# Kernel tuning notes

Measured on AMD Instinct MI355X. Metric: run time of the kernel, lower is better.

## Reference

```python
import jax, jax.numpy as jnp
import numpy as np
import math

B, T, C = 4, 2048, 1024
N_HEAD = 16
HEAD = C // N_HEAD  # 64
ROPE_BASE = 10000.0


def rotate_half(x):
    x1, x2 = x[..., : x.shape[-1] // 2], x[..., x.shape[-1] // 2:]
    return jnp.concatenate((-x2, x1), axis=-1)


def rope_cos_sin(seq_len, dim, dtype=jnp.float32):
    inv_freq = 1.0 / (ROPE_BASE ** (jnp.arange(0, dim, 2, dtype=jnp.float32) / dim))
    t = jnp.arange(seq_len, dtype=jnp.float32)
    freqs = jnp.einsum('i,j->ij', t, inv_freq)          # [T, dim/2]
    emb = jnp.concatenate((freqs, freqs), axis=-1)       # [T, dim]
    return jnp.cos(emb).astype(dtype), jnp.sin(emb).astype(dtype)


def setup_inputs() -> dict:
    key = jax.random.key(0)
    ks = jax.random.split(key, 5)
    s_in = 1.0 / math.sqrt(C)
    return {
        'x': jax.random.normal(ks[0], (B, T, C), dtype=jnp.float32),
        'W_qkv': jax.random.normal(ks[1], (C, 3 * C), dtype=jnp.float32) * s_in,
        'b_qkv': jnp.zeros((3 * C,), dtype=jnp.float32),
        'W_proj': jax.random.normal(ks[2], (C, C), dtype=jnp.float32) * s_in,
        'b_proj': jnp.zeros((C,), dtype=jnp.float32),
    }


def reference(x, W_qkv, b_qkv, W_proj, b_proj):
    b, t, c = x.shape
    qkv = x @ W_qkv + b_qkv                               # [B,T,3C]
    q, k, v = jnp.split(qkv, 3, axis=-1)
    # [B,T,C] -> [B,H,T,hd]
    def to_heads(u):
        return u.reshape(b, t, N_HEAD, HEAD).transpose(0, 2, 1, 3)
    q, k, v = to_heads(q), to_heads(k), to_heads(v)
    # RoPE
    cos, sin = rope_cos_sin(t, HEAD, x.dtype)             # [T,hd]
    cos = cos[None, None]; sin = sin[None, None]
    q = q * cos + rotate_half(q) * sin
    k = k * cos + rotate_half(k) * sin
    # naive causal attention (materializes [B,H,T,T] like the original)
    att = jnp.einsum('bhqd,bhkd->bhqk', q, k) * (1.0 / math.sqrt(HEAD))
    causal = jnp.tril(jnp.ones((t, t), dtype=bool))
    att = jnp.where(causal[None, None], att, -jnp.inf)
    att = jax.nn.softmax(att, axis=-1)
    y = jnp.einsum('bhqk,bhkd->bhqd', att, v)             # [B,H,T,hd]
    y = y.transpose(0, 2, 1, 3).reshape(b, t, c)
    return y @ W_proj + b_proj
```

## Files before the change

### kernel.cpp

```cpp
#include <hip/hip_runtime.h>
#include <stdint.h>

#define B_  4
#define T_  2048
#define C_  1024
#define NH_ 16
#define HD_ 64
#define BH_ (B_*NH_)
#define M_  (B_*T_)

using f32x4  = __attribute__((ext_vector_type(4))) float;
using f32x16 = __attribute__((ext_vector_type(16))) float;
using bf16x8 = __attribute__((ext_vector_type(8))) short;

__device__ __forceinline__ unsigned short f2bf(float x) {
  union { float f; uint32_t u; } v; v.f = x;
  uint32_t u = v.u;
  return (unsigned short)((u + 0x7FFFu + ((u >> 16) & 1u)) >> 16);
}

__device__ __forceinline__ uint32_t cvtpk(float a, float b) {
  uint32_t r;
  asm("v_cvt_pk_bf16_f32 %0, %1, %2" : "=v"(r) : "v"(a), "v"(b));
  return r;
}

__device__ __forceinline__ void gload16(const void* g, void* l) {
  __builtin_amdgcn_global_load_lds(
      (const __attribute__((address_space(1))) void*)g,
      (__attribute__((address_space(3))) void*)l, 16, 0, 0);
}

#define BAR() do { asm volatile("" ::: "memory"); __builtin_amdgcn_s_barrier(); \
                   asm volatile("" ::: "memory"); } while (0)
#define VMC(N) asm volatile("s_waitcnt vmcnt(" #N ")" ::: "memory")

__global__ __launch_bounds__(256)
void k_prep(const float* __restrict__ x,      unsigned short* __restrict__ xb,
            const float* __restrict__ Wqkv,   unsigned short* __restrict__ WqkvT,
            const float* __restrict__ Wproj,  unsigned short* __restrict__ WprojT,
            float* __restrict__ cosT, float* __restrict__ sinT) {
  __shared__ float tile[32][33];
  const int blk = blockIdx.x;
  const int tid = threadIdx.x;
  if (blk < 8192) {
    int i = (blk * 256 + tid) * 4;
    float4 v = *(const float4*)(x + i);
    ushort4 o;
    o.x = f2bf(v.x); o.y = f2bf(v.y); o.z = f2bf(v.z); o.w = f2bf(v.w);
    *(ushort4*)(xb + i) = o;
    return;
  }
  const int tx = tid & 31, ty = tid >> 5;
  if (blk < 12288) {
    const float* W; unsigned short* WT; int N, local;
    if (blk < 11264) { W = Wqkv;  WT = WqkvT;  N = 3*C_; local = blk - 8192; }
    else             { W = Wproj; WT = WprojT; N = C_;   local = blk - 11264; }
    const int NT = N / 32;
    const int bx = local % NT, by = local / NT;
    #pragma unroll
    for (int i = 0; i < 32; i += 8)
      tile[ty + i][tx] = W[(size_t)(by*32 + ty + i) * N + bx*32 + tx];
    __syncthreads();
    #pragma unroll
    for (int i = 0; i < 32; i += 8)
      WT[(size_t)(bx*32 + ty + i) * C_ + by*32 + tx] = f2bf(tile[tx][ty + i]);
    return;
  }
  {
    int t = (blk - 12288) * 8 + ty;
    float inv = expf(-(float)tx * (9.210340371976184f / 32.0f));
    float f = (float)t * inv;
    cosT[t*32 + tx] = cosf(f);
    sinT[t*32 + tx] = sinf(f);
  }
}

template<int N, int K, int EPI>
__global__ __launch_bounds__(256)
void k_gemm(const unsigned short* __restrict__ Ag,
            const unsigned short* __restrict__ BT,
            const float* __restrict__ bias,
            const float* __restrict__ cosT,
            const float* __restrict__ sinT,
            unsigned short* __restrict__ Qh,
            unsigned short* __restrict__ Kh,
            unsigned short* __restrict__ VhT,
            float* __restrict__ outF) {
  __shared__ alignas(16) unsigned short As[2][128*64];
  __shared__ alignas(16) unsigned short Bs[2][128*64];
  const int tid  = threadIdx.x;
  const int lane = tid & 63;
  const int wv   = tid >> 6;
  const int wm   = wv >> 1, wn = wv & 1;
  const int l15  = lane & 15, l4 = lane >> 4;
  constexpr int GN = (N == 3072) ? 6 : 8;
  const int xcd = (int)blockIdx.x & 7;
  const int loc = (int)blockIdx.x >> 3;
  const int sub = loc / (8*GN);
  const int wit = loc % (8*GN);
  const int m0  = (xcd*8 + wit / GN) * 128;
  const int n0  = (sub*GN + wit % GN) * 128;

  f32x4 acc[4][4] = {};

  const int g0 = l4 ^ (l15 & 7);
  const int g1 = (4 + l4) ^ (l15 & 7);
  const int rowA = wm*64 + l15, rowB = wn*64 + l15;
  const unsigned short* aRd0k0 = &As[0][rowA*64 + g0*8];
  const unsigned short* aRd0k1 = &As[0][rowA*64 + g1*8];
  const unsigned short* aRd1k0 = &As[1][rowA*64 + g0*8];
  const unsigned short* aRd1k1 = &As[1][rowA*64 + g1*8];
  const unsigned short* bRd0k0 = &Bs[0][rowB*64 + g0*8];
  const unsigned short* bRd0k1 = &Bs[0][rowB*64 + g1*8];
  const unsigned short* bRd1k0 = &Bs[1][rowB*64 + g0*8];
  const unsigned short* bRd1k1 = &Bs[1][rowB*64 + g1*8];

  const int srow = wv*8 + (lane >> 3);
  const int sg   = (lane & 7) ^ ((lane >> 3) & 7);
  const int voff = srow*K + sg*8;
  const int aUni = m0*K, bUni = n0*K;
  const int ldsD = wv*512;

#define STG(BUF, KT) do { \
  const int _u = (KT)*64; \
  _Pragma("unroll") for (int it = 0; it < 4; ++it) { \
    gload16(Ag + (aUni + it*(32*K) + _u) + voff, (void*)(&As[BUF][it*2048 + ldsD])); \
    gload16(BT + (bUni + it*(32*K) + _u) + voff, (void*)(&Bs[BUF][it*2048 + ldsD])); \
  } \
} while (0)

#define CMP(AK0, AK1, BK0, BK1) do { \
  bf16x8 afr[4][2], bfr[4][2]; \
  _Pragma("unroll") for (int mi = 0; mi < 4; ++mi) { \
    afr[mi][0] = *(const bf16x8*)((AK0) + mi*1024); \
    afr[mi][1] = *(const bf16x8*)((AK1) + mi*1024); \
    bfr[mi][0] = *(const bf16x8*)((BK0) + mi*1024); \
    bfr[mi][1] = *(const bf16x8*)((BK1) + mi*1024); \
  } \
  __builtin_amdgcn_s_setprio(1); \
  _Pragma("unroll") for (int ks = 0; ks < 2; ++ks) \
  _Pragma("unroll") for (int mi = 0; mi < 4; ++mi) \
  _Pragma("unroll") for (int ni = 0; ni < 4; ++ni) \
    acc[mi][ni] = __builtin_amdgcn_mfma_f32_16x16x32_bf16( \
        afr[mi][ks], bfr[ni][ks], acc[mi][ni], 0, 0, 0); \
  __builtin_amdgcn_s_setprio(0); \
} while (0)

  STG(0, 0);
  #pragma unroll 1
  for (int i = 0; i < K/128; ++i) {
    STG(1, 2*i + 1);
    VMC(8);
    BAR();
    CMP(aRd0k0, aRd0k1, bRd0k0, bRd0k1);
    BAR();
    if (i + 1 < K/128) {
      STG(0, 2*i + 2);
      VMC(8);
    } else {
      VMC(0);
    }
    BAR();
    CMP(aRd1k0, aRd1k1, bRd1k0, bRd1k1);
    BAR();
  }
#undef STG
#undef CMP

  if (EPI == 0) {
    const int ncol = n0 + wn*64;
    const int part = ncol >> 10;
    const int hid  = (ncol & 1023) >> 6;
    unsigned short* dstQK = (part == 0) ? Qh : Kh;
    #pragma unroll
    for (int mi = 0; mi < 4; ++mi) {
      #pragma unroll
      for (int j = 0; j < 4; ++j) {
        int row = m0 + wm*64 + mi*16 + l4*4 + j;
        int bb = row >> 11, tt = row & 2047;
        if (part < 2) {
          size_t base = ((size_t)((bb*NH_ + hid) * T_ + tt)) * HD_;
          #pragma unroll
          for (int ni = 0; ni < 2; ++ni) {
            int d = ni*16 + l15;
            float a1 = acc[mi][ni][j]     + bias[ncol + d];
            float a2 = acc[mi][ni + 2][j] + bias[ncol + d + 32];
            float cv = cosT[tt*32 + d], sv = sinT[tt*32 + d];
            float o1 = a1*cv - a2*sv;
            float o2 = a2*cv + a1*sv;
            if (part == 0) { o1 *= 0.18033688011112042f; o2 *= 0.18033688011112042f; }
            dstQK[base + d]      = f2bf(o1);
            dstQK[base + d + 32] = f2bf(o2);
          }
        } else {
          #pragma unroll
          for (int ni = 0; ni < 4; ++ni) {
            int d = ni*16 + l15;
            float av = acc[mi][ni][j] + bias[ncol + d];
            VhT[((size_t)((bb*NH_ + hid) * HD_ + d)) * T_ + tt] = f2bf(av);
          }
        }
      }
    }
  } else {
    #pragma unroll
    for (int mi = 0; mi < 4; ++mi)
      #pragma unroll
      for (int ni = 0; ni < 4; ++ni)
        #pragma unroll
        for (int j = 0; j < 4; ++j) {
          int row = m0 + wm*64 + mi*16 + l4*4 + j;
          int col = n0 + wn*64 + ni*16 + l15;
          outF[(size_t)row * N + col] = acc[mi][ni][j] + bias[col];
        }
  }
}

#define LDW 72
__global__ __launch_bounds__(256, 3)
void k_attn(const unsigned short* __restrict__ Qh,
            const unsigned short* __restrict__ Kh,
            const unsigned short* __restrict__ VhT,
            unsigned short* __restrict__ Y) {
  __shared__ alignas(16) unsigned short Ks[2][64*LDW];
  __shared__ alignas(16) unsigned short Vs[2][64*LDW];
  const int tid  = threadIdx.x;
  const int lane = tid & 63;
  const int wv   = tid >> 6;
  const int l31  = lane & 31;
  const int h    = lane >> 5;
  const int bh   = blockIdx.x & 63;
  const int qb   = 15 - (blockIdx.x >> 6);
  const int r32  = qb*128 + wv*32;
  const int nt   = 2*qb + 2;
  const int qg   = r32 + l31;

  bf16x8 qf[4];
  #pragma unroll
  for (int i = 0; i < 4; ++i)
    qf[i] = *(const bf16x8*)(Qh + ((size_t)(bh*T_ + qg))*HD_ + i*16 + h*8);

  float m_r = -1e30f, l_r = 0.f;
  f32x16 o[2] = {};

  const int srow  = tid >> 3;
  const int sslot = tid & 7;
  const unsigned short* kSrc0 = Kh  + ((size_t)(bh*T_ + srow))*HD_ + sslot*8;
  const unsigned short* kSrc1 = Kh  + ((size_t)(bh*T_ + 32 + srow))*HD_ + sslot*8;
  const unsigned short* vSrc0 = VhT + ((size_t)(bh*HD_ + srow))*T_ + sslot*8;
  const unsigned short* vSrc1 = VhT + ((size_t)(bh*HD_ + 32 + srow))*T_ + sslot*8;
  const int wOff0 = srow*LDW + sslot*8;
  const int wOff1 = (32 + srow)*LDW + sslot*8;

  uint4 kr0, kr1, vr0, vr1;
  auto ldg = [&](int jt) {
    kr0 = *(const uint4*)(kSrc0 + (size_t)jt*64*HD_);
    kr1 = *(const uint4*)(kSrc1 + (size_t)jt*64*HD_);
    vr0 = *(const uint4*)(vSrc0 + jt*64);
    vr1 = *(const uint4*)(vSrc1 + jt*64);
  };
  auto wst = [&](int buf) {
    *(uint4*)(&Ks[buf][wOff0]) = kr0;
    *(uint4*)(&Ks[buf][wOff1]) = kr1;
    *(uint4*)(&Vs[buf][wOff0]) = vr0;
    *(uint4*)(&Vs[buf][wOff1]) = vr1;
  };

  ldg(0); wst(0);
  __syncthreads();
  int cur = 0;

  for (int jt = 0; jt < nt; ++jt) {
    const bool pf = (jt + 1 < nt);
    if (pf) ldg(jt + 1);

    if (jt*64 <= r32 + 31) {
      const unsigned short* kb_ = &Ks[cur][l31*LDW + h*8];
      const unsigned short* vb_ = &Vs[cur][l31*LDW + h*8];

      f32x16 s[2] = {f32x16{0}, f32x16{0}};
      __builtin_amdgcn_s_setprio(1);
      #pragma unroll
      for (int kb = 0; kb < 2; ++kb)
        #pragma unroll
        for (int i = 0; i < 4; ++i) {
          bf16x8 kf = *(const bf16x8*)(kb_ + kb*32*LDW + i*16);
          s[kb] = __builtin_amdgcn_mfma_f32_32x32x16_bf16(kf, qf[i], s[kb], 0, 0, 0);
        }
      __builtin_amdgcn_s_setprio(0);

      float p[2][16];
      const bool diag = (jt + 1)*64 > r32;
      #pragma unroll
      for (int kb = 0; kb < 2; ++kb)
        #pragma unroll
        for (int r = 0; r < 16; ++r) {
          float v = s[kb][r];
          if (diag) {
            int key = jt*64 + kb*32 + (r & 3) + 8*(r >> 2) + 4*h;
            v = (key > qg) ? -1e30f : v;
          }
          p[kb][r] = v;
        }

      float mx[16];
      #pragma unroll
      for (int r = 0; r < 16; ++r) mx[r] = fmaxf(p[0][r], p[1][r]);
      #pragma unroll
      for (int st = 8; st > 0; st >>= 1)
        #pragma unroll
        for (int r = 0; r < 8; ++r)
          if (r < st) mx[r] = fmaxf(mx[r], mx[r + st]);
      float tm = fmaxf(mx[0], __shfl_xor(mx[0], 32));

      if (!__all(tm <= m_r + 8.0f)) {
        float mn = fmaxf(m_r, tm);
        float scale = exp2f(m_r - mn);
        m_r = mn;
        l_r *= scale;
        #pragma unroll
        for (int dblk = 0; dblk < 2; ++dblk)
          #pragma unroll
          for (int r = 0; r < 16; ++r)
            o[dblk][r] *= scale;
      }

      #pragma unroll
      for (int kb = 0; kb < 2; ++kb)
        #pragma unroll
        for (int r = 0; r < 16; ++r)
          p[kb][r] = exp2f(p[kb][r] - m_r);

      float sm[16];
      #pragma unroll
      for (int r = 0; r < 16; ++r) sm[r] = p[0][r] + p[1][r];
      #pragma unroll
      for (int st = 8; st > 0; st >>= 1)
        #pragma unroll
        for (int r = 0; r < 8; ++r)
          if (r < st) sm[r] += sm[r + st];
      l_r += sm[0] + __shfl_xor(sm[0], 32);

      #pragma unroll
      for (int kb = 0; kb < 2; ++kb) {
        uint32_t a01 = cvtpk(p[kb][0],  p[kb][1]);
        uint32_t a23 = cvtpk(p[kb][2],  p[kb][3]);
        uint32_t a45 = cvtpk(p[kb][4],  p[kb][5]);
        uint32_t a67 = cvtpk(p[kb][6],  p[kb][7]);
        uint32_t b01 = cvtpk(p[kb][8],  p[kb][9]);
        uint32_t b23 = cvtpk(p[kb][10], p[kb][11]);
        uint32_t b45 = cvtpk(p[kb][12], p[kb][13]);
        uint32_t b67 = cvtpk(p[kb][14], p[kb][15]);
        uint32_t s1 = h ? a01 : a45, s2 = h ? a23 : a67;
        uint32_t s3 = h ? b01 : b45, s4 = h ? b23 : b67;
        uint32_t x1 = __shfl_xor(s1, 32), x2 = __shfl_xor(s2, 32);
        uint32_t x3 = __shfl_xor(s3, 32), x4 = __shfl_xor(s4, 32);
        union { bf16x8 v; uint32_t d[4]; } f0, f1;
        f0.d[0] = h ? x1 : a01;  f0.d[1] = h ? x2 : a23;
        f0.d[2] = h ? a45 : x1;  f0.d[3] = h ? a67 : x2;
        f1.d[0] = h ? x3 : b01;  f1.d[1] = h ? x4 : b23;
        f1.d[2] = h ? b45 : x3;  f1.d[3] = h ? b67 : x4;

        __builtin_amdgcn_s_setprio(1);
        #pragma unroll
        for (int koff = 0; koff < 2; ++koff) {
          bf16x8 pf = koff ? f1.v : f0.v;
          #pragma unroll
          for (int dblk = 0; dblk < 2; ++dblk) {
            bf16x8 vf = *(const bf16x8*)(vb_ + dblk*32*LDW + kb*32 + koff*16);
            o[dblk] = __builtin_amdgcn_mfma_f32_32x32x16_bf16(vf, pf, o[dblk], 0, 0, 0);
          }
        }
        __builtin_amdgcn_s_setprio(0);
      }
    }

    if (pf) wst(cur ^ 1);
    __syncthreads();
    cur ^= 1;
  }

  int b = bh >> 4, hd = bh & 15;
  float rinv = 1.0f / l_r;
  unsigned short* yrow = Y + ((size_t)(b*T_ + r32 + l31))*C_ + hd*64;
  #pragma unroll
  for (int dblk = 0; dblk < 2; ++dblk)
    #pragma unroll
    for (int g2 = 0; g2 < 4; ++g2) {
      ushort4 o4;
      o4.x = f2bf(o[dblk][g2*4 + 0] * rinv);
      o4.y = f2bf(o[dblk][g2*4 + 1] * rinv);
      o4.z = f2bf(o[dblk][g2*4 + 2] * rinv);
      o4.w = f2bf(o[dblk][g2*4 + 3] * rinv);
      *(ushort4*)(yrow + dblk*32 + g2*8 + 4*h) = o4;
    }
}


extern "C" void kernel_launch(void* const* d_in, const int* in_sizes, int n_in,
                              void* d_out, int out_size, void* d_ws, size_t ws_size,
                              hipStream_t stream) {
  const float* x      = (const float*)d_in[0];
  const float* W_qkv  = (const float*)d_in[1];
  const float* b_qkv  = (const float*)d_in[2];
  const float* W_proj = (const float*)d_in[3];
  const float* b_proj = (const float*)d_in[4];
  float* out = (float*)d_out;

  char* ws = (char*)d_ws;
  size_t off = 0;
  auto alloc = [&](size_t bytes) {
    void* p = ws + off; off += (bytes + 255) & ~(size_t)255; return p;
  };
  unsigned short* xb     = (unsigned short*)alloc((size_t)M_ * C_ * 2);
  unsigned short* WqkvT  = (unsigned short*)alloc((size_t)3 * C_ * C_ * 2);
  unsigned short* WprojT = (unsigned short*)alloc((size_t)C_ * C_ * 2);
  unsigned short* Qh     = (unsigned short*)alloc((size_t)M_ * C_ * 2);
  unsigned short* Kh     = (unsigned short*)alloc((size_t)M_ * C_ * 2);
  unsigned short* VhT    = (unsigned short*)alloc((size_t)M_ * C_ * 2);
  float* cosT = (float*)alloc((size_t)T_ * 32 * 4);
  float* sinT = (float*)alloc((size_t)T_ * 32 * 4);
  unsigned short* Y = xb;

  k_prep<<<dim3(12544), 256, 0, stream>>>(x, xb, W_qkv, WqkvT, W_proj, WprojT,
                                          cosT, sinT);

  k_gemm<3*C_, C_, 0><<<dim3(1536), 256, 0, stream>>>(
      xb, WqkvT, b_qkv, cosT, sinT, Qh, Kh, VhT, nullptr);

  k_attn<<<dim3(T_/128 * BH_), 256, 0, stream>>>(Qh, Kh, VhT, Y);

  k_gemm<C_, C_, 1><<<dim3(512), 256, 0, stream>>>(
      Y, WprojT, b_proj, nullptr, nullptr, nullptr, nullptr, nullptr, out);
}
```

Measured before the change: 188.4 us.

## Enlarge attention KV tile to 128 keys per iteration

```diff
diff --git a/kernel.cpp b/kernel.cpp
--- a/kernel.cpp
+++ b/kernel.cpp
@@ -217,14 +217,15 @@
   }
 }
 
-#define LDW 72
-__global__ __launch_bounds__(256, 3)
+#define LDWK 72
+#define LDWV 136
+__global__ __launch_bounds__(256, 2)
 void k_attn(const unsigned short* __restrict__ Qh,
             const unsigned short* __restrict__ Kh,
             const unsigned short* __restrict__ VhT,
             unsigned short* __restrict__ Y) {
-  __shared__ alignas(16) unsigned short Ks[2][64*LDW];
-  __shared__ alignas(16) unsigned short Vs[2][64*LDW];
+  __shared__ alignas(16) unsigned short Ks[2][128*LDWK];
+  __shared__ alignas(16) unsigned short Vs[2][64*LDWV];
   const int tid  = threadIdx.x;
   const int lane = tid & 63;
   const int wv   = tid >> 6;
@@ -233,7 +234,7 @@
   const int bh   = blockIdx.x & 63;
   const int qb   = 15 - (blockIdx.x >> 6);
   const int r32  = qb*128 + wv*32;
-  const int nt   = 2*qb + 2;
+  const int nt   = qb + 1;
   const int qg   = r32 + l31;
 
   bf16x8 qf[4];
@@ -246,25 +247,27 @@
 
   const int srow  = tid >> 3;
   const int sslot = tid & 7;
-  const unsigned short* kSrc0 = Kh  + ((size_t)(bh*T_ + srow))*HD_ + sslot*8;
-  const unsigned short* kSrc1 = Kh  + ((size_t)(bh*T_ + 32 + srow))*HD_ + sslot*8;
-  const unsigned short* vSrc0 = VhT + ((size_t)(bh*HD_ + srow))*T_ + sslot*8;
-  const unsigned short* vSrc1 = VhT + ((size_t)(bh*HD_ + 32 + srow))*T_ + sslot*8;
-  const int wOff0 = srow*LDW + sslot*8;
-  const int wOff1 = (32 + srow)*LDW + sslot*8;
-
-  uint4 kr0, kr1, vr0, vr1;
+  const unsigned short* kSrc = Kh + ((size_t)(bh*T_ + srow))*HD_ + sslot*8;
+  const int kOff = srow*LDWK + sslot*8;
+  const int vd    = tid >> 2;
+  const int vslot = tid & 3;
+  const unsigned short* vSrc = VhT + ((size_t)(bh*HD_ + vd))*T_ + vslot*8;
+  const int vOff = vd*LDWV + vslot*8;
+
+  uint4 kr[4], vr[4];
   auto ldg = [&](int jt) {
-    kr0 = *(const uint4*)(kSrc0 + (size_t)jt*64*HD_);
-    kr1 = *(const uint4*)(kSrc1 + (size_t)jt*64*HD_);
-    vr0 = *(const uint4*)(vSrc0 + jt*64);
-    vr1 = *(const uint4*)(vSrc1 + jt*64);
+    #pragma unroll
+    for (int c = 0; c < 4; ++c) {
+      kr[c] = *(const uint4*)(kSrc + ((size_t)jt*128 + c*32)*HD_);
+      vr[c] = *(const uint4*)(vSrc + jt*128 + c*32);
+    }
   };
   auto wst = [&](int buf) {
-    *(uint4*)(&Ks[buf][wOff0]) = kr0;
-    *(uint4*)(&Ks[buf][wOff1]) = kr1;
-    *(uint4*)(&Vs[buf][wOff0]) = vr0;
-    *(uint4*)(&Vs[buf][wOff1]) = vr1;
+    #pragma unroll
+    for (int c = 0; c < 4; ++c) {
+      *(uint4*)(&Ks[buf][kOff + c*32*LDWK]) = kr[c];
+      *(uint4*)(&Vs[buf][vOff + c*32])      = vr[c];
+    }
   };
 
   ldg(0); wst(0);
@@ -275,106 +278,100 @@
     const bool pf = (jt + 1 < nt);
     if (pf) ldg(jt + 1);
 
-    if (jt*64 <= r32 + 31) {
-      const unsigned short* kb_ = &Ks[cur][l31*LDW + h*8];
-      const unsigned short* vb_ = &Vs[cur][l31*LDW + h*8];
-
-      f32x16 s[2] = {f32x16{0}, f32x16{0}};
-      __builtin_amdgcn_s_setprio(1);
-      #pragma unroll
-      for (int kb = 0; kb < 2; ++kb)
-        #pragma unroll
-        for (int i = 0; i < 4; ++i) {
-          bf16x8 kf = *(const bf16x8*)(kb_ + kb*32*LDW + i*16);
-          s[kb] = __builtin_amdgcn_mfma_f32_32x32x16_bf16(kf, qf[i], s[kb], 0, 0, 0);
-        }
-      __builtin_amdgcn_s_setprio(0);
-
-      float p[2][16];
-      const bool diag = (jt + 1)*64 > r32;
-      #pragma unroll
-      for (int kb = 0; kb < 2; ++kb)
+    const unsigned short* kb_ = &Ks[cur][l31*LDWK + h*8];
+    const unsigned short* vb_ = &Vs[cur][l31*LDWV + h*8];
+
+    f32x16 s[4] = {f32x16{0}, f32x16{0}, f32x16{0}, f32x16{0}};
+    __builtin_amdgcn_s_setprio(1);
+    #pragma unroll
+    for (int kb = 0; kb < 4; ++kb)
+      #pragma unroll
+      for (int i = 0; i < 4; ++i) {
+        bf16x8 kf = *(const bf16x8*)(kb_ + kb*32*LDWK + i*16);
+        s[kb] = __builtin_amdgcn_mfma_f32_32x32x16_bf16(kf, qf[i], s[kb], 0, 0, 0);
+      }
+    __builtin_amdgcn_s_setprio(0);
+
+    if (jt == qb) {
+      #pragma unroll
+      for (int kb = 0; kb < 4; ++kb)
         #pragma unroll
         for (int r = 0; r < 16; ++r) {
-          float v = s[kb][r];
-          if (diag) {
-            int key = jt*64 + kb*32 + (r & 3) + 8*(r >> 2) + 4*h;
-            v = (key > qg) ? -1e30f : v;
-          }
-          p[kb][r] = v;
+          int key = jt*128 + kb*32 + (r & 3) + 8*(r >> 2) + 4*h;
+          if (key > qg) s[kb][r] = -1e30f;
         }
-
-      float mx[16];
-      #pragma unroll
-      for (int r = 0; r < 16; ++r) mx[r] = fmaxf(p[0][r], p[1][r]);
-      #pragma unroll
-      for (int st = 8; st > 0; st >>= 1)
-        #pragma unroll
-        for (int r = 0; r < 8; ++r)
-          if (r < st) mx[r] = fmaxf(mx[r], mx[r + st]);
-      float tm = fmaxf(mx[0], __shfl_xor(mx[0], 32));
-
-      if (!__all(tm <= m_r + 8.0f)) {
-        float mn = fmaxf(m_r, tm);
-        float scale = exp2f(m_r - mn);
-        m_r = mn;
-        l_r *= scale;
-        #pragma unroll
-        for (int dblk = 0; dblk < 2; ++dblk)
-          #pragma unroll
-          for (int r = 0; r < 16; ++r)
-            o[dblk][r] *= scale;
-      }
-
-      #pragma unroll
-      for (int kb = 0; kb < 2; ++kb)
+    }
+
+    float mx[16];
+    #pragma unroll
+    for (int r = 0; r < 16; ++r)
+      mx[r] = fmaxf(fmaxf(s[0][r], s[1][r]), fmaxf(s[2][r], s[3][r]));
+    #pragma unroll
+    for (int st = 8; st > 0; st >>= 1)
+      #pragma unroll
+      for (int r = 0; r < 8; ++r)
+        if (r < st) mx[r] = fmaxf(mx[r], mx[r + st]);
+    float tm = fmaxf(mx[0], __shfl_xor(mx[0], 32));
+
+    if (!__all(tm <= m_r + 8.0f)) {
+      float mn = fmaxf(m_r, tm);
+      float scale = exp2f(m_r - mn);
+      m_r = mn;
+      l_r *= scale;
+      #pragma unroll
+      for (int dblk = 0; dblk < 2; ++dblk)
         #pragma unroll
         for (int r = 0; r < 16; ++r)
-          p[kb][r] = exp2f(p[kb][r] - m_r);
-
+          o[dblk][r] *= scale;
+    }
+
+    float lacc = 0.f;
+    #pragma unroll
+    for (int kb = 0; kb < 4; ++kb) {
+      float p[16];
+      #pragma unroll
+      for (int r = 0; r < 16; ++r) p[r] = exp2f(s[kb][r] - m_r);
       float sm[16];
       #pragma unroll
-      for (int r = 0; r < 16; ++r) sm[r] = p[0][r] + p[1][r];
+      for (int r = 0; r < 16; ++r) sm[r] = p[r];
       #pragma unroll
       for (int st = 8; st > 0; st >>= 1)
         #pragma unroll
         for (int r = 0; r < 8; ++r)
           if (r < st) sm[r] += sm[r + st];
-      l_r += sm[0] + __shfl_xor(sm[0], 32);
-
-      #pragma unroll
-      for (int kb = 0; kb < 2; ++kb) {
-        uint32_t a01 = cvtpk(p[kb][0],  p[kb][1]);
-        uint32_t a23 = cvtpk(p[kb][2],  p[kb][3]);
-        uint32_t a45 = cvtpk(p[kb][4],  p[kb][5]);
-        uint32_t a67 = cvtpk(p[kb][6],  p[kb][7]);
-        uint32_t b01 = cvtpk(p[kb][8],  p[kb][9]);
-        uint32_t b23 = cvtpk(p[kb][10], p[kb][11]);
-        uint32_t b45 = cvtpk(p[kb][12], p[kb][13]);
-        uint32_t b67 = cvtpk(p[kb][14], p[kb][15]);
-        uint32_t s1 = h ? a01 : a45, s2 = h ? a23 : a67;
-        uint32_t s3 = h ? b01 : b45, s4 = h ? b23 : b67;
-        uint32_t x1 = __shfl_xor(s1, 32), x2 = __shfl_xor(s2, 32);
-        uint32_t x3 = __shfl_xor(s3, 32), x4 = __shfl_xor(s4, 32);
-        union { bf16x8 v; uint32_t d[4]; } f0, f1;
-        f0.d[0] = h ? x1 : a01;  f0.d[1] = h ? x2 : a23;
-        f0.d[2] = h ? a45 : x1;  f0.d[3] = h ? a67 : x2;
-        f1.d[0] = h ? x3 : b01;  f1.d[1] = h ? x4 : b23;
-        f1.d[2] = h ? b45 : x3;  f1.d[3] = h ? b67 : x4;
-
-        __builtin_amdgcn_s_setprio(1);
+      lacc += sm[0];
+
+      uint32_t a01 = cvtpk(p[0],  p[1]);
+      uint32_t a23 = cvtpk(p[2],  p[3]);
+      uint32_t a45 = cvtpk(p[4],  p[5]);
+      uint32_t a67 = cvtpk(p[6],  p[7]);
+      uint32_t b01 = cvtpk(p[8],  p[9]);
+      uint32_t b23 = cvtpk(p[10], p[11]);
+      uint32_t b45 = cvtpk(p[12], p[13]);
+      uint32_t b67 = cvtpk(p[14], p[15]);
+      uint32_t s1 = h ? a01 : a45, s2 = h ? a23 : a67;
+      uint32_t s3 = h ? b01 : b45, s4 = h ? b23 : b67;
+      uint32_t x1 = __shfl_xor(s1, 32), x2 = __shfl_xor(s2, 32);
+      uint32_t x3 = __shfl_xor(s3, 32), x4 = __shfl_xor(s4, 32);
+      union { bf16x8 v; uint32_t d[4]; } f0, f1;
+      f0.d[0] = h ? x1 : a01;  f0.d[1] = h ? x2 : a23;
+      f0.d[2] = h ? a45 : x1;  f0.d[3] = h ? a67 : x2;
+      f1.d[0] = h ? x3 : b01;  f1.d[1] = h ? x4 : b23;
+      f1.d[2] = h ? b45 : x3;  f1.d[3] = h ? b67 : x4;
+
+      __builtin_amdgcn_s_setprio(1);
+      #pragma unroll
+      for (int koff = 0; koff < 2; ++koff) {
+        bf16x8 pfv = koff ? f1.v : f0.v;
         #pragma unroll
-        for (int koff = 0; koff < 2; ++koff) {
-          bf16x8 pf = koff ? f1.v : f0.v;
-          #pragma unroll
-          for (int dblk = 0; dblk < 2; ++dblk) {
-            bf16x8 vf = *(const bf16x8*)(vb_ + dblk*32*LDW + kb*32 + koff*16);
-            o[dblk] = __builtin_amdgcn_mfma_f32_32x32x16_bf16(vf, pf, o[dblk], 0, 0, 0);
-          }
+        for (int dblk = 0; dblk < 2; ++dblk) {
+          bf16x8 vf = *(const bf16x8*)(vb_ + dblk*32*LDWV + kb*32 + koff*16);
+          o[dblk] = __builtin_amdgcn_mfma_f32_32x32x16_bf16(vf, pfv, o[dblk], 0, 0, 0);
         }
-        __builtin_amdgcn_s_setprio(0);
       }
-    }
+      __builtin_amdgcn_s_setprio(0);
+    }
+    l_r += lacc + __shfl_xor(lacc, 32);
 
     if (pf) wst(cur ^ 1);
     __syncthreads();
```

After: 237.8 us. +26.2%, slower.
